# Kernel tuning notes

Measured on AMD Instinct MI355X. Metric: run time of the kernel, lower is better.

The kernel has to match this reference:

```python
import jax, jax.numpy as jnp
import numpy as np
from jax import lax

NB, D_MODEL, D_INNER, D_STATE, K, L, BATCH, NCLS, DT_RANK = 3, 512, 1024, 8, 4, 2048, 4, 10, 32


def setup_inputs() -> dict:
    key = jax.random.key(0)
    ks = jax.random.split(key, 12)
    s = 0.02
    inp = {
        "x": jax.random.normal(ks[0], (BATCH, L, D_MODEL), jnp.float32),
        "in_proj_w": s * jax.random.normal(ks[1], (NB, D_MODEL, 2 * D_INNER), jnp.float32),
        "conv_w": s * jax.random.normal(ks[2], (NB, D_INNER, K), jnp.float32),
        "conv_b": jnp.zeros((NB, D_INNER), jnp.float32),
        "x_proj_w": s * jax.random.normal(ks[3], (NB, D_INNER, DT_RANK + 2 * D_STATE), jnp.float32),
        "dt_proj_w": s * jax.random.normal(ks[4], (NB, DT_RANK, D_INNER), jnp.float32),
        "dt_proj_b": jnp.full((NB, D_INNER), -4.0, jnp.float32),
        "A_log": jnp.broadcast_to(jnp.log(jnp.arange(1, D_STATE + 1, dtype=jnp.float32)), (NB, D_INNER, D_STATE)).copy(),
        "D": jnp.ones((NB, D_INNER), jnp.float32),
        "out_proj_w": s * jax.random.normal(ks[5], (NB, D_INNER, D_MODEL), jnp.float32),
        "cls_w": s * jax.random.normal(ks[6], (D_MODEL, NCLS), jnp.float32),
        "cls_b": jnp.zeros((NCLS,), jnp.float32),
    }
    return inp


def _mamba_block(x, Wi, cw, cb, Wx, Wdt, bdt, A_log, Dp, Wo):
    # x: [B, L, d_model]
    Bsz, Lx, _ = x.shape
    d_inner = Dp.shape[0]
    d_state = A_log.shape[-1]
    dt_rank = Wdt.shape[0]
    xz = x @ Wi                               # [B, L, 2*d_inner]
    u, z = jnp.split(xz, 2, axis=-1)
    # causal depthwise conv1d over time
    uc = jnp.swapaxes(u, 1, 2)                # [B, d_inner, L]
    k = cw.shape[-1]
    uc = lax.conv_general_dilated(uc, cw[:, None, :], window_strides=(1,),
                                  padding=[(k - 1, 0)], feature_group_count=d_inner,
                                  dimension_numbers=("NCH", "OIH", "NCH"))
    u = jax.nn.silu(jnp.swapaxes(uc, 1, 2) + cb)   # [B, L, d_inner]
    dbl = u @ Wx                                   # [B, L, dt_rank + 2*d_state]
    dt = dbl[..., :dt_rank]
    Bm = dbl[..., dt_rank:dt_rank + d_state]
    Cm = dbl[..., dt_rank + d_state:]
    delta = jax.nn.softplus(dt @ Wdt + bdt)        # [B, L, d_inner]
    A = -jnp.exp(A_log)                            # [d_inner, d_state]

    def step(h, inp):
        d_t, B_t, C_t, u_t = inp                   # [B,d],[B,n],[B,n],[B,d]
        h = jnp.exp(d_t[..., None] * A) * h + (d_t * u_t)[..., None] * B_t[:, None, :]
        return h, jnp.einsum("bdn,bn->bd", h, C_t)

    xs = (jnp.swapaxes(delta, 0, 1), jnp.swapaxes(Bm, 0, 1),
          jnp.swapaxes(Cm, 0, 1), jnp.swapaxes(u, 0, 1))
    h0 = jnp.zeros((Bsz, d_inner, d_state), x.dtype)
    _, ys = lax.scan(step, h0, xs)                 # ys: [L, B, d_inner]
    y = jnp.swapaxes(ys, 0, 1) + u * Dp
    y = y * jax.nn.silu(z)
    return x + y @ Wo                              # residual


def reference(x, in_proj_w, conv_w, conv_b, x_proj_w, dt_proj_w, dt_proj_b, A_log, D, out_proj_w, cls_w, cls_b):
    nb = in_proj_w.shape[0]
    for i in range(nb):
        x = _mamba_block(x, in_proj_w[i], conv_w[i], conv_b[i], x_proj_w[i],
                         dt_proj_w[i], dt_proj_b[i], A_log[i], D[i], out_proj_w[i])
    pooled = jnp.mean(x, axis=1)                   # AdaptiveAvgPool1d(1) over seq
    return pooled @ cls_w + cls_b                  # [B, num_classes]
```

## Files before the change

### kernel.cpp

```cpp
#include <hip/hip_runtime.h>
#include <cstddef>
#include <cstdint>

#define L_SEQ   2048
#define BATCH_N 4
#define DMODEL  512
#define DINNER  1024
#define DSTATE  8
#define KCONV   4
#define DTRANK  32
#define NBLK    3
#define NCLS_N  10
#define MROWS   (BATCH_N * L_SEQ)
#define DBLW    48
#define NSPLIT  8

#define LC2 16
#define NC2 (L_SEQ / LC2)
#define DHALF (DINNER / 2)
#define SCAN_THREADS 512
#define SCAN_WAVES   (SCAN_THREADS / 64)

#define CGRP 8
#define CPG  (NC2 / CGRP)

typedef __attribute__((ext_vector_type(8))) short bf16x8;
typedef __attribute__((ext_vector_type(4))) short bf16x4;
typedef __attribute__((ext_vector_type(2))) short bf16x2;
typedef __attribute__((ext_vector_type(4))) float f32x4;

__device__ __forceinline__ float sigmoid_fast(float x) { return 1.f / (1.f + __expf(-x)); }
__device__ __forceinline__ float silu_fast(float x)    { return x * sigmoid_fast(x); }
__device__ __forceinline__ float softplus_fast(float x){
    return fmaxf(x, 0.f) + __logf(1.f + __expf(-fabsf(x)));
}
__device__ __forceinline__ float exp2_fast(float x) {
#if __has_builtin(__builtin_amdgcn_exp2f)
    return __builtin_amdgcn_exp2f(x);
#else
    return __expf(x * 0.69314718055994531f);
#endif
}
#define LOG2E 1.44269504088896341f

__device__ __forceinline__ unsigned short f2bf(float f) {
    union { float f; uint32_t u; } v; v.f = f;
    const uint32_t u = v.u;
    return (unsigned short)((u + 0x7fffu + ((u >> 16) & 1u)) >> 16);
}
__device__ __forceinline__ float bf2f(unsigned short h) {
    union { uint32_t u; float f; } v; v.u = ((uint32_t)h) << 16;
    return v.f;
}
__device__ __forceinline__ float bf2f_s(short h) { return bf2f((unsigned short)h); }

__device__ __forceinline__ void load_lds16(const void* g, void* l) {
    __builtin_amdgcn_global_load_lds(
        (const __attribute__((address_space(1))) unsigned int*)g,
        (__attribute__((address_space(3))) unsigned int*)l,
        16, 0, 0);
}

template <int K, int NT, int EPI>
__global__ __launch_bounds__(256) void gemm_bf16(
    const unsigned short* __restrict__ A, int lda,
    const unsigned short* __restrict__ Bt, int ldb,
    int ldc,
    unsigned short* __restrict__ Obf,
    float* __restrict__ pool)
{
    constexpr int BCH   = NT / 8;
    constexpr int NTW   = NT / 32;
    constexpr int STAGE = 8192 + NT * 64;
    constexpr int EPIL  = 128 * (NT + 8);
    constexpr int SMEM  = (STAGE > EPIL) ? STAGE : EPIL;
    __shared__ unsigned short sMem[SMEM];
    unsigned short* sA = sMem;
    unsigned short* sB = sMem + 8192;

    const int tid  = threadIdx.x;
    const int lane = tid & 63;
    const int wave = tid >> 6;
    const int m0 = blockIdx.y * 128;
    const int n0 = blockIdx.x * NT;
    const int wm = (wave >> 1) * 64;
    const int wn = (wave & 1) * (NT / 2);
    const int lm = lane & 15;
    const int lq = lane >> 4;

    const int srow = lane >> 3;
    const int scol = ((lane & 7) ^ srow) * 8;

    f32x4 acc[4][NTW];
    #pragma unroll
    for (int i = 0; i < 4; ++i)
        #pragma unroll
        for (int j = 0; j < NTW; ++j) acc[i][j] = (f32x4){0.f, 0.f, 0.f, 0.f};

    for (int k0 = 0; k0 < K; k0 += 64) {
        #pragma unroll
        for (int c = wave; c < 16; c += 4)
            load_lds16(A + (size_t)(m0 + c * 8 + srow) * lda + k0 + scol, &sA[c * 512]);
        #pragma unroll
        for (int c = wave; c < BCH; c += 4)
            load_lds16(Bt + (size_t)(n0 + c * 8 + srow) * ldb + k0 + scol, &sB[c * 512]);
        __syncthreads();
        #pragma unroll
        for (int ks = 0; ks < 2; ++ks) {
            bf16x8 aF[4], bF[NTW];
            #pragma unroll
            for (int mt = 0; mt < 4; ++mt) {
                const int row = wm + mt * 16 + lm;
                aF[mt] = *(const bf16x8*)&sA[row * 64 + (((ks * 4 + lq) ^ (lm & 7)) * 8)];
            }
            #pragma unroll
            for (int nt = 0; nt < NTW; ++nt) {
                const int row = wn + nt * 16 + lm;
                bF[nt] = *(const bf16x8*)&sB[row * 64 + (((ks * 4 + lq) ^ (lm & 7)) * 8)];
            }
            #pragma unroll
            for (int mt = 0; mt < 4; ++mt)
                #pragma unroll
                for (int nt = 0; nt < NTW; ++nt)
                    acc[mt][nt] = __builtin_amdgcn_mfma_f32_16x16x32_bf16(
                        aF[mt], bF[nt], acc[mt][nt], 0, 0, 0);
        }
        __syncthreads();
    }

    unsigned short* sOut = sMem;
    #pragma unroll
    for (int mt = 0; mt < 4; ++mt) {
        #pragma unroll
        for (int nt = 0; nt < NTW; ++nt) {
            #pragma unroll
            for (int r = 0; r < 4; ++r) {
                const int row = wm + mt * 16 + lq * 4 + r;
                const int col = wn + nt * 16 + lm;
                float v = acc[mt][nt][r];
                if (EPI >= 2) {
                    const size_t gi = (size_t)(m0 + row) * ldc + n0 + col;
                    v += bf2f(Obf[gi]);
                }
                sOut[row * (NT + 8) + col] = f2bf(v);
            }
        }
    }
    __syncthreads();
    #pragma unroll
    for (int j = 0; j < NT / 16; ++j) {
        const int idx = j * 256 + tid;
        const int row = idx / (NT / 8);
        const int cpos = (idx % (NT / 8)) * 8;
        *(bf16x8*)&Obf[(size_t)(m0 + row) * ldc + n0 + cpos] =
            *(const bf16x8*)&sOut[row * (NT + 8) + cpos];
    }
    if (EPI == 3) {
        const int b = m0 >> 11;
        const int col = tid & (NT - 1);
        const int q = tid / NT;
        constexpr int RPQ = 128 / (256 / NT);
        float s = 0.f;
        #pragma unroll
        for (int r = q * RPQ; r < (q + 1) * RPQ; ++r)
            s += bf2f(sOut[r * (NT + 8) + col]);
        atomicAdd(&pool[b * DMODEL + n0 + col], s);
    }
}

__global__ __launch_bounds__(256) void gemm_xproj(
    const unsigned short* __restrict__ ub,
    const unsigned short* __restrict__ Wxt,
    float* __restrict__ Xp)
{
    const int tid = threadIdx.x, lane = tid & 63, wave = tid >> 6;
    const int lm = lane & 15, lq = lane >> 4;
    const int rowA = blockIdx.x * 128 + wave * 32;
    const int split = blockIdx.y;
    const int k0 = split * (DINNER / NSPLIT);

    f32x4 acc[2][3];
    #pragma unroll
    for (int i = 0; i < 2; ++i)
        #pragma unroll
        for (int j = 0; j < 3; ++j) acc[i][j] = (f32x4){0.f, 0.f, 0.f, 0.f};

    #pragma unroll
    for (int kk = 0; kk < DINNER / NSPLIT; kk += 32) {
        const int k = k0 + kk;
        bf16x8 aF[2], bF[3];
        #pragma unroll
        for (int mt = 0; mt < 2; ++mt)
            aF[mt] = *(const bf16x8*)&ub[(size_t)(rowA + mt * 16 + lm) * DINNER + k + lq * 8];
        #pragma unroll
        for (int nt = 0; nt < 3; ++nt)
            bF[nt] = *(const bf16x8*)&Wxt[(size_t)(nt * 16 + lm) * DINNER + k + lq * 8];
        #pragma unroll
        for (int mt = 0; mt < 2; ++mt)
            #pragma unroll
            for (int nt = 0; nt < 3; ++nt)
                acc[mt][nt] = __builtin_amdgcn_mfma_f32_16x16x32_bf16(
                    aF[mt], bF[nt], acc[mt][nt], 0, 0, 0);
    }
    float* dst = Xp + (size_t)split * MROWS * DBLW;
    #pragma unroll
    for (int mt = 0; mt < 2; ++mt)
        #pragma unroll
        for (int nt = 0; nt < 3; ++nt)
            #pragma unroll
            for (int r = 0; r < 4; ++r)
                dst[(size_t)(rowA + mt * 16 + lq * 4 + r) * DBLW
                    + nt * 16 + lm] = acc[mt][nt][r];
}

__global__ __launch_bounds__(256) void xp_reduce(
    const float* __restrict__ Xp, float* __restrict__ dblsum)
{
    const int i = blockIdx.x * 256 + threadIdx.x;
    f32x4 s = (f32x4){0.f, 0.f, 0.f, 0.f};
    #pragma unroll
    for (int sp = 0; sp < NSPLIT; ++sp)
        s += ((const f32x4*)(Xp + (size_t)sp * MROWS * DBLW))[i];
    ((f32x4*)dblsum)[i] = s;
}

__global__ void prep_negA(const float* __restrict__ A_log, float* __restrict__ negA) {
    const int i = blockIdx.x * 256 + threadIdx.x;
    if (i < NBLK * DINNER * DSTATE)
        negA[i] = -__expf(A_log[i]) * LOG2E;
}

__global__ __launch_bounds__(256) void transpose_cast(
    const float* __restrict__ in, unsigned short* __restrict__ out,
    int Kdim, int Ndim, size_t in_stride, size_t out_stride)
{
    __shared__ float s[32][33];
    const float* ip = in + blockIdx.z * in_stride;
    unsigned short* op = out + blockIdx.z * out_stride;
    const int bx = blockIdx.x * 32;
    const int by = blockIdx.y * 32;
    const int t = threadIdx.x;
    const int r = t >> 3;
    const int c4 = (t & 7) * 4;

    const int row = by + r;
    if (bx + c4 + 3 < Ndim) {
        float4 v = *(const float4*)&ip[(size_t)row * Ndim + bx + c4];
        s[r][c4 + 0] = v.x; s[r][c4 + 1] = v.y; s[r][c4 + 2] = v.z; s[r][c4 + 3] = v.w;
    } else {
        for (int i = 0; i < 4; ++i) {
            const int col = bx + c4 + i;
            s[r][c4 + i] = (col < Ndim) ? ip[(size_t)row * Ndim + col] : 0.f;
        }
    }
    __syncthreads();
    if (bx + r < Ndim) {
        unsigned short w0 = f2bf(s[c4 + 0][r]), w1 = f2bf(s[c4 + 1][r]);
        unsigned short w2 = f2bf(s[c4 + 2][r]), w3 = f2bf(s[c4 + 3][r]);
        uint2 pk;
        pk.x = (uint32_t)w0 | ((uint32_t)w1 << 16);
        pk.y = (uint32_t)w2 | ((uint32_t)w3 << 16);
        *(uint2*)&op[(size_t)(bx + r) * Kdim + by + c4] = pk;
    }
}

__global__ void cast_init(const float* __restrict__ in, unsigned short* __restrict__ outb,
                          float* __restrict__ pooled_accum, int n4) {
    const int i = blockIdx.x * 256 + threadIdx.x;
    if (i < BATCH_N * DMODEL / 4)
        ((f32x4*)pooled_accum)[i] = (f32x4){0.f, 0.f, 0.f, 0.f};
    if (i >= n4) return;
    float4 v = ((const float4*)in)[i];
    uint2 pk;
    pk.x = (uint32_t)f2bf(v.x) | ((uint32_t)f2bf(v.y) << 16);
    pk.y = (uint32_t)f2bf(v.z) | ((uint32_t)f2bf(v.w) << 16);
    ((uint2*)outb)[i] = pk;
}

__global__ void conv_w_transpose(const float* __restrict__ cw, float* __restrict__ cwt) {
    const int i = blockIdx.x * 256 + threadIdx.x;
    if (i >= NBLK * DINNER * KCONV) return;
    const int blk = i >> 12;
    const int rem = i & 4095;
    const int d = rem >> 2;
    const int k = rem & 3;
    cwt[blk * 4096 + k * DINNER + d] = cw[blk * 4096 + d * KCONV + k];
}

__global__ __launch_bounds__(256) void conv_silu_kernel(
    const unsigned short* __restrict__ xz,
    const float* __restrict__ cwt,
    const float* __restrict__ cb,
    unsigned short* __restrict__ ub)
{
    const int idx = blockIdx.x * 256 + threadIdx.x;
    const int dv = idx & 127;
    const int m  = idx >> 7;
    const int t  = m & (L_SEQ - 1);
    const int d0 = dv * 8;

    float acc[8];
    {
        float4 c0 = *(const float4*)&cb[d0];
        float4 c1 = *(const float4*)&cb[d0 + 4];
        acc[0] = c0.x; acc[1] = c0.y; acc[2] = c0.z; acc[3] = c0.w;
        acc[4] = c1.x; acc[5] = c1.y; acc[6] = c1.z; acc[7] = c1.w;
    }
    #pragma unroll
    for (int k = 0; k < KCONV; ++k) {
        const int tt = t + k - (KCONV - 1);
        if (tt >= 0) {
            bf16x8 xv = *(const bf16x8*)&xz[(size_t)(m - t + tt) * (2 * DINNER) + d0];
            float4 w0 = *(const float4*)&cwt[k * DINNER + d0];
            float4 w1 = *(const float4*)&cwt[k * DINNER + d0 + 4];
            acc[0] = fmaf(bf2f_s(xv[0]), w0.x, acc[0]);
            acc[1] = fmaf(bf2f_s(xv[1]), w0.y, acc[1]);
            acc[2] = fmaf(bf2f_s(xv[2]), w0.z, acc[2]);
            acc[3] = fmaf(bf2f_s(xv[3]), w0.w, acc[3]);
            acc[4] = fmaf(bf2f_s(xv[4]), w1.x, acc[4]);
            acc[5] = fmaf(bf2f_s(xv[5]), w1.y, acc[5]);
            acc[6] = fmaf(bf2f_s(xv[6]), w1.z, acc[6]);
            acc[7] = fmaf(bf2f_s(xv[7]), w1.w, acc[7]);
        }
    }
    bf16x8 o;
    #pragma unroll
    for (int j = 0; j < 8; ++j) o[j] = (short)f2bf(silu_fast(acc[j]));
    *(bf16x8*)&ub[(size_t)m * DINNER + d0] = o;
}

__device__ __forceinline__ void dt_recompute_lds(
    unsigned short* sDelta,
    const float* __restrict__ dblsum,
    const unsigned short* __restrict__ Wdtt,
    const float* __restrict__ bdt,
    size_t m0, int lane, int wave, int dbase)
{
    const int lm = lane & 15, lq = lane >> 4;
    bf16x8 aF;
    {
        const float* p = &dblsum[(m0 + lm) * DBLW + lq * 8];
        float4 x0 = *(const float4*)p;
        float4 x1 = *(const float4*)(p + 4);
        aF[0] = (short)f2bf(x0.x); aF[1] = (short)f2bf(x0.y);
        aF[2] = (short)f2bf(x0.z); aF[3] = (short)f2bf(x0.w);
        aF[4] = (short)f2bf(x1.x); aF[5] = (short)f2bf(x1.y);
        aF[6] = (short)f2bf(x1.z); aF[7] = (short)f2bf(x1.w);
    }
    constexpr int NPW = DHALF / (16 * SCAN_WAVES);
    #pragma unroll
    for (int nt = 0; nt < NPW; ++nt) {
        const int cloc = wave * (DHALF / SCAN_WAVES) + nt * 16;
        const int col16 = dbase + cloc;
        bf16x8 bF = *(const bf16x8*)&Wdtt[(size_t)(col16 + lm) * DTRANK + lq * 8];
        f32x4 acc = (f32x4){0.f, 0.f, 0.f, 0.f};
        acc = __builtin_amdgcn_mfma_f32_16x16x32_bf16(aF, bF, acc, 0, 0, 0);
        const float bias = bdt[col16 + lm];
        #pragma unroll
        for (int r = 0; r < 4; ++r)
            sDelta[(lq * 4 + r) * DHALF + cloc + lm] =
                f2bf(softplus_fast(acc[r] + bias));
    }
}

__global__ __launch_bounds__(SCAN_THREADS) void scan_chunk_kernel(
    const unsigned short* __restrict__ ub,
    const float* __restrict__ dblsum,
    const unsigned short* __restrict__ Wdtt,
    const float* __restrict__ bdt,
    const float* __restrict__ negA,
    float* __restrict__ PSbuf)
{
    const int c  = blockIdx.x;
    const int dh = blockIdx.y;
    const int b  = blockIdx.z;
    const int tid = threadIdx.x;
    const int lane = tid & 63;
    const int wave = tid >> 6;
    const int dbase = dh * DHALF;
    const int d = dbase + tid;

    __shared__ unsigned short sDelta[LC2 * DHALF];
    __shared__ float sB[LC2][DSTATE];

    const size_t m0 = (size_t)b * L_SEQ + c * LC2;

    dt_recompute_lds(sDelta, dblsum, Wdtt, bdt, m0, lane, wave, dbase);
    if (tid < LC2 * DSTATE) {
        const int r = tid >> 3, n = tid & 7;
        sB[r][n] = dblsum[(m0 + r) * DBLW + DTRANK + n];
    }
    __syncthreads();

    float a[DSTATE], S[DSTATE];
    {
        float4 a0 = *(const float4*)&negA[(size_t)d * DSTATE];
        float4 a1 = *(const float4*)&negA[(size_t)d * DSTATE + 4];
        a[0] = a0.x; a[1] = a0.y; a[2] = a0.z; a[3] = a0.w;
        a[4] = a1.x; a[5] = a1.y; a[6] = a1.z; a[7] = a1.w;
    }
    #pragma unroll
    for (int n = 0; n < DSTATE; ++n) S[n] = 0.f;
    float dtsum = 0.f;

    for (int r = 0; r < LC2; ++r) {
        const size_t m = m0 + r;
        const float dt = bf2f(sDelta[r * DHALF + tid]);
        const float du = dt * bf2f(ub[m * DINNER + d]);
        dtsum += dt;
        #pragma unroll
        for (int n = 0; n < DSTATE; ++n) {
            const float e = exp2_fast(dt * a[n]);
            S[n] = fmaf(e, S[n], du * sB[r][n]);
        }
    }

    const size_t nb = (size_t)(b * NC2 + c) * DSTATE;
    #pragma unroll
    for (int n = 0; n < DSTATE; ++n) {
        float2 ps;
        ps.x = exp2_fast(a[n] * dtsum);
        ps.y = S[n];
        *(float2*)&PSbuf[(nb + n) * (DINNER * 2) + (size_t)d * 2] = ps;
    }
}

__global__ __launch_bounds__(512) void scan_combine_kernel(
    const float* __restrict__ PSbuf,
    float* __restrict__ Hbuf)
{
    const int dl = threadIdx.x & 63;
    const int g  = threadIdx.x >> 6;
    const int d  = blockIdx.x * 64 + dl;
    const int n  = blockIdx.y;
    const int b  = blockIdx.z;

    __shared__ float sP[CGRP][64];
    __shared__ float sS[CGRP][64];

    const int c0 = g * CPG;
    float Pseg = 1.f, Sseg = 0.f;
    #pragma unroll 4
    for (int cc = 0; cc < CPG; ++cc) {
        const size_t row = (size_t)(b * NC2 + c0 + cc) * DSTATE + n;
        const float2 ps = *(const float2*)&PSbuf[row * (DINNER * 2) + (size_t)d * 2];
        Pseg *= ps.x;
        Sseg = fmaf(ps.x, Sseg, ps.y);
    }
    sP[g][dl] = Pseg;
    sS[g][dl] = Sseg;
    __syncthreads();

    float h = 0.f;
    for (int gg = 0; gg < g; ++gg)
        h = fmaf(sP[gg][dl], h, sS[gg][dl]);

    #pragma unroll 4
    for (int cc = 0; cc < CPG; ++cc) {
        const size_t row = (size_t)(b * NC2 + c0 + cc) * DSTATE + n;
        const float2 ps = *(const float2*)&PSbuf[row * (DINNER * 2) + (size_t)d * 2];
        Hbuf[row * DINNER + d] = h;
        h = fmaf(ps.x, h, ps.y);
    }
}

__global__ __launch_bounds__(SCAN_THREADS) void scan_out_kernel(
    const unsigned short* __restrict__ ub,
    const float* __restrict__ dblsum,
    const unsigned short* __restrict__ Wdtt,
    const float* __restrict__ bdt,
    const unsigned short* __restrict__ xz,
    const float* __restrict__ negA,
    const float* __restrict__ Dp,
    const float* __restrict__ Hin,
    unsigned short* __restrict__ ybuf)
{
    const int c  = blockIdx.x;
    const int dh = blockIdx.y;
    const int b  = blockIdx.z;
    const int tid = threadIdx.x;
    const int lane = tid & 63;
    const int wave = tid >> 6;
    const int dbase = dh * DHALF;
    const int d = dbase + tid;

    __shared__ unsigned short sDelta[LC2 * DHALF];
    __shared__ float sB[LC2][DSTATE];
    __shared__ float sC[LC2][DSTATE];

    const size_t m0 = (size_t)b * L_SEQ + c * LC2;

    dt_recompute_lds(sDelta, dblsum, Wdtt, bdt, m0, lane, wave, dbase);
    if (tid < LC2 * 2 * DSTATE) {
        const int r = tid >> 4, j = tid & 15;
        const float v = dblsum[(m0 + r) * DBLW + DTRANK + j];
        if (j < DSTATE) sB[r][j] = v;
        else            sC[r][j - DSTATE] = v;
    }
    __syncthreads();

    float a[DSTATE], h[DSTATE];
    {
        float4 a0 = *(const float4*)&negA[(size_t)d * DSTATE];
        float4 a1 = *(const float4*)&negA[(size_t)d * DSTATE + 4];
        a[0] = a0.x; a[1] = a0.y; a[2] = a0.z; a[3] = a0.w;
        a[4] = a1.x; a[5] = a1.y; a[6] = a1.z; a[7] = a1.w;
    }
    const size_t base = ((size_t)(b * NC2 + c) * DSTATE) * DINNER + d;
    #pragma unroll
    for (int n = 0; n < DSTATE; ++n)
        h[n] = Hin[base + (size_t)n * DINNER];
    const float Dd = Dp[d];

    for (int r = 0; r < LC2; ++r) {
        const size_t m = m0 + r;
        const float dt = bf2f(sDelta[r * DHALF + tid]);
        const float ut = bf2f(ub[m * DINNER + d]);
        const float zt = bf2f(xz[m * (2 * DINNER) + DINNER + d]);
        const float du = dt * ut;
        float acc = 0.f;
        #pragma unroll
        for (int n = 0; n < DSTATE; ++n) {
            const float e = exp2_fast(dt * a[n]);
            h[n] = fmaf(e, h[n], du * sB[r][n]);
            acc = fmaf(h[n], sC[r][n], acc);
        }
        ybuf[m * DINNER + d] = f2bf(fmaf(ut, Dd, acc) * silu_fast(zt));
    }
}

__global__ __launch_bounds__(512) void pool_cls_kernel(
    const float* __restrict__ pooled_accum,
    const float* __restrict__ w,
    const float* __restrict__ bias,
    float* __restrict__ out)
{
    __shared__ float sp[DMODEL];
    const int b = blockIdx.x;
    const int dm = threadIdx.x;
    sp[dm] = pooled_accum[b * DMODEL + dm] * (1.f / (float)L_SEQ);
    __syncthreads();
    if (dm < NCLS_N) {
        float acc = bias[dm];
        for (int k = 0; k < DMODEL; ++k)
            acc = fmaf(sp[k], w[k * NCLS_N + dm], acc);
        out[b * NCLS_N + dm] = acc;
    }
}

extern "C" void kernel_launch(void* const* d_in, const int* in_sizes, int n_in,
                              void* d_out, int out_size, void* d_ws, size_t ws_size,
                              hipStream_t stream) {
    const float* x_in      = (const float*)d_in[0];
    const float* in_proj_w = (const float*)d_in[1];
    const float* conv_w    = (const float*)d_in[2];
    const float* conv_b    = (const float*)d_in[3];
    const float* x_proj_w  = (const float*)d_in[4];
    const float* dt_proj_w = (const float*)d_in[5];
    const float* dt_proj_b = (const float*)d_in[6];
    const float* A_log     = (const float*)d_in[7];
    const float* Dp        = (const float*)d_in[8];
    const float* out_proj_w= (const float*)d_in[9];
    const float* cls_w     = (const float*)d_in[10];
    const float* cls_b     = (const float*)d_in[11];
    float* out = (float*)d_out;

    char* w = (char*)d_ws;
    auto alloc = [&](size_t bytes) { char* p = w; w += (bytes + 255) & ~(size_t)255; return p; };
    unsigned short* xz_bf  = (unsigned short*)alloc((size_t)MROWS * 2 * DINNER * 2);
    unsigned short* ub     = (unsigned short*)alloc((size_t)MROWS * DINNER * 2);
    float*          Xp     = (float*)         alloc((size_t)NSPLIT * MROWS * DBLW * 4);
    float*          dblsum = (float*)         alloc((size_t)MROWS * DBLW * 4);
    float*          PSbuf  = (float*)         alloc((size_t)BATCH_N * NC2 * DSTATE * DINNER * 2 * 4);
    float*          Hbuf   = (float*)         alloc((size_t)BATCH_N * NC2 * DSTATE * DINNER * 4);
    unsigned short* xb     = (unsigned short*)alloc((size_t)MROWS * DMODEL * 2);
    unsigned short* ybuf   = (unsigned short*)alloc((size_t)MROWS * DINNER * 2);
    unsigned short* Wit    = (unsigned short*)alloc((size_t)NBLK * 2048 * 512 * 2);
    unsigned short* Wot    = (unsigned short*)alloc((size_t)NBLK * 512 * 1024 * 2);
    unsigned short* Wxt    = (unsigned short*)alloc((size_t)NBLK * DBLW * 1024 * 2);
    unsigned short* Wdtt   = (unsigned short*)alloc((size_t)NBLK * 1024 * DTRANK * 2);
    float*          cwt    = (float*)         alloc((size_t)NBLK * KCONV * DINNER * 4);
    float*          negA   = (float*)         alloc((size_t)NBLK * DINNER * DSTATE * 4);
    float*          pooled = (float*)         alloc((size_t)BATCH_N * DMODEL * 4);

    cast_init<<<(MROWS * DMODEL / 4) / 256, 256, 0, stream>>>(
        x_in, xb, pooled, MROWS * DMODEL / 4);
    transpose_cast<<<dim3(2048 / 32, 512 / 32, NBLK), 256, 0, stream>>>(
        in_proj_w, Wit, 512, 2048, (size_t)512 * 2048, (size_t)2048 * 512);
    transpose_cast<<<dim3(512 / 32, 1024 / 32, NBLK), 256, 0, stream>>>(
        out_proj_w, Wot, 1024, 512, (size_t)1024 * 512, (size_t)512 * 1024);
    transpose_cast<<<dim3(2, 1024 / 32, NBLK), 256, 0, stream>>>(
        x_proj_w, Wxt, 1024, DBLW, (size_t)1024 * DBLW, (size_t)DBLW * 1024);
    transpose_cast<<<dim3(1024 / 32, 1, NBLK), 256, 0, stream>>>(
        dt_proj_w, Wdtt, DTRANK, 1024, (size_t)DTRANK * 1024, (size_t)1024 * DTRANK);
    conv_w_transpose<<<(NBLK * DINNER * KCONV + 255) / 256, 256, 0, stream>>>(conv_w, cwt);
    prep_negA<<<(NBLK * DINNER * DSTATE + 255) / 256, 256, 0, stream>>>(A_log, negA);

    for (int blk = 0; blk < NBLK; ++blk) {
        const unsigned short* Wit_b  = Wit  + (size_t)blk * 2048 * 512;
        const unsigned short* Wot_b  = Wot  + (size_t)blk * 512 * 1024;
        const unsigned short* Wxt_b  = Wxt  + (size_t)blk * DBLW * 1024;
        const unsigned short* Wdtt_b = Wdtt + (size_t)blk * 1024 * DTRANK;
        const float* cwt_b = cwt + (size_t)blk * KCONV * DINNER;
        const float* cb  = conv_b    + (size_t)blk * DINNER;
        const float* bdt = dt_proj_b + (size_t)blk * DINNER;
        const float* nA  = negA      + (size_t)blk * DINNER * DSTATE;
        const float* Dv  = Dp        + (size_t)blk * DINNER;

        gemm_bf16<512, 128, 0><<<dim3(2048 / 128, MROWS / 128), 256, 0, stream>>>(
            xb, DMODEL, Wit_b, DMODEL, 2 * DINNER, xz_bf, nullptr);
        conv_silu_kernel<<<(MROWS * 128) / 256, 256, 0, stream>>>(
            xz_bf, cwt_b, cb, ub);
        gemm_xproj<<<dim3(MROWS / 128, NSPLIT), 256, 0, stream>>>(ub, Wxt_b, Xp);
        xp_reduce<<<(MROWS * DBLW / 4) / 256, 256, 0, stream>>>(Xp, dblsum);
        {
            dim3 gridA(NC2, 2, BATCH_N);
            scan_chunk_kernel<<<gridA, SCAN_THREADS, 0, stream>>>(
                ub, dblsum, Wdtt_b, bdt, nA, PSbuf);
            scan_combine_kernel<<<dim3(DINNER / 64, DSTATE, BATCH_N), 512, 0, stream>>>(
                PSbuf, Hbuf);
            scan_out_kernel<<<gridA, SCAN_THREADS, 0, stream>>>(
                ub, dblsum, Wdtt_b, bdt, xz_bf, nA, Dv, Hbuf, ybuf);
        }
        if (blk < NBLK - 1)
            gemm_bf16<1024, 64, 2><<<dim3(DMODEL / 64, MROWS / 128), 256, 0, stream>>>(
                ybuf, DINNER, Wot_b, DINNER, DMODEL, xb, nullptr);
        else
            gemm_bf16<1024, 64, 3><<<dim3(DMODEL / 64, MROWS / 128), 256, 0, stream>>>(
                ybuf, DINNER, Wot_b, DINNER, DMODEL, xb, pooled);
    }

    pool_cls_kernel<<<BATCH_N, DMODEL, 0, stream>>>(pooled, cls_w, cls_b, out);
}
```

Measured before the change: 521.5 us.

## Fuse chunked scan, combine and output passes into one cooperative kernel

Merges the three scan kernels (chunk summary, cross-chunk combine, output) into a single cooperative launch separated by grid-wide syncs. The delta recompute and B/C loads into LDS now happen once instead of twice, and the u values are kept in registers between phases. This removes two kernel launches and the repeated delta GEMM and global reloads. In exchange, the whole 1024-block grid must be co-resident (launch bounds raised to 8 blocks per CU), grid syncs add latency, and the combine phase runs on only half the blocks.

```diff
diff --git a/kernel.cpp b/kernel.cpp
--- a/kernel.cpp
+++ b/kernel.cpp
@@ -1,6 +1,9 @@
 #include <hip/hip_runtime.h>
+#include <hip/hip_cooperative_groups.h>
 #include <cstddef>
 #include <cstdint>
+
+namespace cg = cooperative_groups;
 
 #define L_SEQ   2048
 #define BATCH_N 4
@@ -363,13 +366,17 @@
     }
 }
 
-__global__ __launch_bounds__(SCAN_THREADS) void scan_chunk_kernel(
+__global__ __launch_bounds__(SCAN_THREADS, 8) void scan_fused(
     const unsigned short* __restrict__ ub,
     const float* __restrict__ dblsum,
     const unsigned short* __restrict__ Wdtt,
     const float* __restrict__ bdt,
+    const unsigned short* __restrict__ xz,
     const float* __restrict__ negA,
-    float* __restrict__ PSbuf)
+    const float* __restrict__ Dp,
+    float* __restrict__ PSbuf,
+    float* __restrict__ Hbuf,
+    unsigned short* __restrict__ ybuf)
 {
     const int c  = blockIdx.x;
     const int dh = blockIdx.y;
@@ -382,111 +389,9 @@
 
     __shared__ unsigned short sDelta[LC2 * DHALF];
     __shared__ float sB[LC2][DSTATE];
-
-    const size_t m0 = (size_t)b * L_SEQ + c * LC2;
-
-    dt_recompute_lds(sDelta, dblsum, Wdtt, bdt, m0, lane, wave, dbase);
-    if (tid < LC2 * DSTATE) {
-        const int r = tid >> 3, n = tid & 7;
-        sB[r][n] = dblsum[(m0 + r) * DBLW + DTRANK + n];
-    }
-    __syncthreads();
-
-    float a[DSTATE], S[DSTATE];
-    {
-        float4 a0 = *(const float4*)&negA[(size_t)d * DSTATE];
-        float4 a1 = *(const float4*)&negA[(size_t)d * DSTATE + 4];
-        a[0] = a0.x; a[1] = a0.y; a[2] = a0.z; a[3] = a0.w;
-        a[4] = a1.x; a[5] = a1.y; a[6] = a1.z; a[7] = a1.w;
-    }
-    #pragma unroll
-    for (int n = 0; n < DSTATE; ++n) S[n] = 0.f;
-    float dtsum = 0.f;
-
-    for (int r = 0; r < LC2; ++r) {
-        const size_t m = m0 + r;
-        const float dt = bf2f(sDelta[r * DHALF + tid]);
-        const float du = dt * bf2f(ub[m * DINNER + d]);
-        dtsum += dt;
-        #pragma unroll
-        for (int n = 0; n < DSTATE; ++n) {
-            const float e = exp2_fast(dt * a[n]);
-            S[n] = fmaf(e, S[n], du * sB[r][n]);
-        }
-    }
-
-    const size_t nb = (size_t)(b * NC2 + c) * DSTATE;
-    #pragma unroll
-    for (int n = 0; n < DSTATE; ++n) {
-        float2 ps;
-        ps.x = exp2_fast(a[n] * dtsum);
-        ps.y = S[n];
-        *(float2*)&PSbuf[(nb + n) * (DINNER * 2) + (size_t)d * 2] = ps;
-    }
-}
-
-__global__ __launch_bounds__(512) void scan_combine_kernel(
-    const float* __restrict__ PSbuf,
-    float* __restrict__ Hbuf)
-{
-    const int dl = threadIdx.x & 63;
-    const int g  = threadIdx.x >> 6;
-    const int d  = blockIdx.x * 64 + dl;
-    const int n  = blockIdx.y;
-    const int b  = blockIdx.z;
-
+    __shared__ float sC[LC2][DSTATE];
     __shared__ float sP[CGRP][64];
     __shared__ float sS[CGRP][64];
-
-    const int c0 = g * CPG;
-    float Pseg = 1.f, Sseg = 0.f;
-    #pragma unroll 4
-    for (int cc = 0; cc < CPG; ++cc) {
-        const size_t row = (size_t)(b * NC2 + c0 + cc) * DSTATE + n;
-        const float2 ps = *(const float2*)&PSbuf[row * (DINNER * 2) + (size_t)d * 2];
-        Pseg *= ps.x;
-        Sseg = fmaf(ps.x, Sseg, ps.y);
-    }
-    sP[g][dl] = Pseg;
-    sS[g][dl] = Sseg;
-    __syncthreads();
-
-    float h = 0.f;
-    for (int gg = 0; gg < g; ++gg)
-        h = fmaf(sP[gg][dl], h, sS[gg][dl]);
-
-    #pragma unroll 4
-    for (int cc = 0; cc < CPG; ++cc) {
-        const size_t row = (size_t)(b * NC2 + c0 + cc) * DSTATE + n;
-        const float2 ps = *(const float2*)&PSbuf[row * (DINNER * 2) + (size_t)d * 2];
-        Hbuf[row * DINNER + d] = h;
-        h = fmaf(ps.x, h, ps.y);
-    }
-}
-
-__global__ __launch_bounds__(SCAN_THREADS) void scan_out_kernel(
-    const unsigned short* __restrict__ ub,
-    const float* __restrict__ dblsum,
-    const unsigned short* __restrict__ Wdtt,
-    const float* __restrict__ bdt,
-    const unsigned short* __restrict__ xz,
-    const float* __restrict__ negA,
-    const float* __restrict__ Dp,
-    const float* __restrict__ Hin,
-    unsigned short* __restrict__ ybuf)
-{
-    const int c  = blockIdx.x;
-    const int dh = blockIdx.y;
-    const int b  = blockIdx.z;
-    const int tid = threadIdx.x;
-    const int lane = tid & 63;
-    const int wave = tid >> 6;
-    const int dbase = dh * DHALF;
-    const int d = dbase + tid;
-
-    __shared__ unsigned short sDelta[LC2 * DHALF];
-    __shared__ float sB[LC2][DSTATE];
-    __shared__ float sC[LC2][DSTATE];
 
     const size_t m0 = (size_t)b * L_SEQ + c * LC2;
 
@@ -499,33 +404,104 @@
     }
     __syncthreads();
 
-    float a[DSTATE], h[DSTATE];
+    float a[DSTATE];
     {
         float4 a0 = *(const float4*)&negA[(size_t)d * DSTATE];
         float4 a1 = *(const float4*)&negA[(size_t)d * DSTATE + 4];
         a[0] = a0.x; a[1] = a0.y; a[2] = a0.z; a[3] = a0.w;
         a[4] = a1.x; a[5] = a1.y; a[6] = a1.z; a[7] = a1.w;
     }
-    const size_t base = ((size_t)(b * NC2 + c) * DSTATE) * DINNER + d;
-    #pragma unroll
-    for (int n = 0; n < DSTATE; ++n)
-        h[n] = Hin[base + (size_t)n * DINNER];
-    const float Dd = Dp[d];
-
-    for (int r = 0; r < LC2; ++r) {
-        const size_t m = m0 + r;
-        const float dt = bf2f(sDelta[r * DHALF + tid]);
-        const float ut = bf2f(ub[m * DINNER + d]);
-        const float zt = bf2f(xz[m * (2 * DINNER) + DINNER + d]);
-        const float du = dt * ut;
-        float acc = 0.f;
+
+    uint32_t upk[LC2 / 2];
+    {
+        float S[DSTATE];
+        #pragma unroll
+        for (int n = 0; n < DSTATE; ++n) S[n] = 0.f;
+        float dtsum = 0.f;
+        for (int r = 0; r < LC2; ++r) {
+            const size_t m = m0 + r;
+            const unsigned short ubits = ub[m * DINNER + d];
+            if (r & 1) upk[r >> 1] |= ((uint32_t)ubits << 16);
+            else       upk[r >> 1]  = (uint32_t)ubits;
+            const float dt = bf2f(sDelta[r * DHALF + tid]);
+            const float du = dt * bf2f(ubits);
+            dtsum += dt;
+            #pragma unroll
+            for (int n = 0; n < DSTATE; ++n) {
+                const float e = exp2_fast(dt * a[n]);
+                S[n] = fmaf(e, S[n], du * sB[r][n]);
+            }
+        }
+        const size_t nb = (size_t)(b * NC2 + c) * DSTATE;
         #pragma unroll
         for (int n = 0; n < DSTATE; ++n) {
-            const float e = exp2_fast(dt * a[n]);
-            h[n] = fmaf(e, h[n], du * sB[r][n]);
-            acc = fmaf(h[n], sC[r][n], acc);
-        }
-        ybuf[m * DINNER + d] = f2bf(fmaf(ut, Dd, acc) * silu_fast(zt));
+            float2 ps;
+            ps.x = exp2_fast(a[n] * dtsum);
+            ps.y = S[n];
+            *(float2*)&PSbuf[(nb + n) * (DINNER * 2) + (size_t)d * 2] = ps;
+        }
+    }
+
+    cg::this_grid().sync();
+
+    {
+        const int flat = c + NC2 * (dh + 2 * b);
+        if (flat < 512) {
+            const int bx = flat & 15;
+            const int n2 = (flat >> 4) & 7;
+            const int b2 = flat >> 7;
+            const int dl = tid & 63;
+            const int g  = tid >> 6;
+            const int dd = bx * 64 + dl;
+            const int c0 = g * CPG;
+            float Pseg = 1.f, Sseg = 0.f;
+            #pragma unroll 4
+            for (int cc = 0; cc < CPG; ++cc) {
+                const size_t row = (size_t)(b2 * NC2 + c0 + cc) * DSTATE + n2;
+                const float2 ps = *(const float2*)&PSbuf[row * (DINNER * 2) + (size_t)dd * 2];
+                Pseg *= ps.x;
+                Sseg = fmaf(ps.x, Sseg, ps.y);
+            }
+            sP[g][dl] = Pseg;
+            sS[g][dl] = Sseg;
+            __syncthreads();
+            float h = 0.f;
+            for (int gg = 0; gg < g; ++gg)
+                h = fmaf(sP[gg][dl], h, sS[gg][dl]);
+            #pragma unroll 4
+            for (int cc = 0; cc < CPG; ++cc) {
+                const size_t row = (size_t)(b2 * NC2 + c0 + cc) * DSTATE + n2;
+                const float2 ps = *(const float2*)&PSbuf[row * (DINNER * 2) + (size_t)dd * 2];
+                Hbuf[row * DINNER + dd] = h;
+                h = fmaf(ps.x, h, ps.y);
+            }
+        }
+    }
+
+    cg::this_grid().sync();
+
+    {
+        float h[DSTATE];
+        const size_t base = ((size_t)(b * NC2 + c) * DSTATE) * DINNER + d;
+        #pragma unroll
+        for (int n = 0; n < DSTATE; ++n)
+            h[n] = Hbuf[base + (size_t)n * DINNER];
+        const float Dd = Dp[d];
+        for (int r = 0; r < LC2; ++r) {
+            const size_t m = m0 + r;
+            const float dt = bf2f(sDelta[r * DHALF + tid]);
+            const float ut = bf2f((unsigned short)((upk[r >> 1] >> ((r & 1) * 16)) & 0xffffu));
+            const float zt = bf2f(xz[m * (2 * DINNER) + DINNER + d]);
+            const float du = dt * ut;
+            float acc = 0.f;
+            #pragma unroll
+            for (int n = 0; n < DSTATE; ++n) {
+                const float e = exp2_fast(dt * a[n]);
+                h[n] = fmaf(e, h[n], du * sB[r][n]);
+                acc = fmaf(h[n], sC[r][n], acc);
+            }
+            ybuf[m * DINNER + d] = f2bf(fmaf(ut, Dd, acc) * silu_fast(zt));
+        }
     }
 }
 
@@ -614,13 +590,21 @@
         gemm_xproj<<<dim3(MROWS / 128, NSPLIT), 256, 0, stream>>>(ub, Wxt_b, Xp);
         xp_reduce<<<(MROWS * DBLW / 4) / 256, 256, 0, stream>>>(Xp, dblsum);
         {
-            dim3 gridA(NC2, 2, BATCH_N);
-            scan_chunk_kernel<<<gridA, SCAN_THREADS, 0, stream>>>(
-                ub, dblsum, Wdtt_b, bdt, nA, PSbuf);
-            scan_combine_kernel<<<dim3(DINNER / 64, DSTATE, BATCH_N), 512, 0, stream>>>(
-                PSbuf, Hbuf);
-            scan_out_kernel<<<gridA, SCAN_THREADS, 0, stream>>>(
-                ub, dblsum, Wdtt_b, bdt, xz_bf, nA, Dv, Hbuf, ybuf);
+            const unsigned short* ub_p   = ub;
+            const float*          dbl_p  = dblsum;
+            const unsigned short* wdtt_p = Wdtt_b;
+            const float*          bdt_p  = bdt;
+            const unsigned short* xz_p   = xz_bf;
+            const float*          na_p   = nA;
+            const float*          dp_p   = Dv;
+            float*                ps_p   = PSbuf;
+            float*                h_p    = Hbuf;
+            unsigned short*       y_p    = ybuf;
+            void* kargs[] = {&ub_p, &dbl_p, &wdtt_p, &bdt_p, &xz_p,
+                             &na_p, &dp_p, &ps_p, &h_p, &y_p};
+            hipLaunchCooperativeKernel((const void*)scan_fused,
+                                       dim3(NC2, 2, BATCH_N), dim3(SCAN_THREADS),
+                                       kargs, 0, stream);
         }
         if (blk < NBLK - 1)
             gemm_bf16<1024, 64, 2><<<dim3(DMODEL / 64, MROWS / 128), 256, 0, stream>>>(
```

Measured after the change: 1.297 ms. 2.49x slower.

## Remap GEMM workgroups per XCD and halve xproj tile rows

Applied to the files above, without the earlier changes.

The main bf16 GEMM now remaps its flat workgroup index so that consecutive tiles land on the same XCD (MI355X dispatches workgroups round-robin across 8 XCDs). The aim is better L2 reuse of shared A/B panels. Separately, gemm_xproj now uses 16 rows per wave instead of 32 and launches twice as many blocks, trading register reuse of B fragments for more parallelism and occupancy. The remap assumes the round-robin dispatch order and adds a little index arithmetic.

```diff
diff --git a/kernel.cpp b/kernel.cpp
--- a/kernel.cpp
+++ b/kernel.cpp
@@ -81,8 +81,18 @@
     const int tid  = threadIdx.x;
     const int lane = tid & 63;
     const int wave = tid >> 6;
-    const int m0 = blockIdx.y * 128;
-    const int n0 = blockIdx.x * NT;
+
+    const int nwgx = gridDim.x;
+    const int nwg  = nwgx * gridDim.y;
+    int flat = blockIdx.y * nwgx + blockIdx.x;
+    {
+        const int q = nwg >> 3, r = nwg & 7;
+        const int xcd = flat & 7, lid = flat >> 3;
+        flat = (xcd < r ? xcd * (q + 1) : r * (q + 1) + (xcd - r) * q) + lid;
+    }
+    const int m0 = (flat / nwgx) * 128;
+    const int n0 = (flat % nwgx) * NT;
+
     const int wm = (wave >> 1) * 64;
     const int wn = (wave & 1) * (NT / 2);
     const int lm = lane & 15;
@@ -175,42 +185,33 @@
 {
     const int tid = threadIdx.x, lane = tid & 63, wave = tid >> 6;
     const int lm = lane & 15, lq = lane >> 4;
-    const int rowA = blockIdx.x * 128 + wave * 32;
+    const int rowA = blockIdx.x * 64 + wave * 16;
     const int split = blockIdx.y;
     const int k0 = split * (DINNER / NSPLIT);
 
-    f32x4 acc[2][3];
-    #pragma unroll
-    for (int i = 0; i < 2; ++i)
-        #pragma unroll
-        for (int j = 0; j < 3; ++j) acc[i][j] = (f32x4){0.f, 0.f, 0.f, 0.f};
+    f32x4 acc[3];
+    #pragma unroll
+    for (int j = 0; j < 3; ++j) acc[j] = (f32x4){0.f, 0.f, 0.f, 0.f};
 
     #pragma unroll
     for (int kk = 0; kk < DINNER / NSPLIT; kk += 32) {
         const int k = k0 + kk;
-        bf16x8 aF[2], bF[3];
-        #pragma unroll
-        for (int mt = 0; mt < 2; ++mt)
-            aF[mt] = *(const bf16x8*)&ub[(size_t)(rowA + mt * 16 + lm) * DINNER + k + lq * 8];
+        bf16x8 aF = *(const bf16x8*)&ub[(size_t)(rowA + lm) * DINNER + k + lq * 8];
+        bf16x8 bF[3];
         #pragma unroll
         for (int nt = 0; nt < 3; ++nt)
             bF[nt] = *(const bf16x8*)&Wxt[(size_t)(nt * 16 + lm) * DINNER + k + lq * 8];
         #pragma unroll
-        for (int mt = 0; mt < 2; ++mt)
-            #pragma unroll
-            for (int nt = 0; nt < 3; ++nt)
-                acc[mt][nt] = __builtin_amdgcn_mfma_f32_16x16x32_bf16(
-                    aF[mt], bF[nt], acc[mt][nt], 0, 0, 0);
+        for (int nt = 0; nt < 3; ++nt)
+            acc[nt] = __builtin_amdgcn_mfma_f32_16x16x32_bf16(
+                aF, bF[nt], acc[nt], 0, 0, 0);
     }
     float* dst = Xp + (size_t)split * MROWS * DBLW;
     #pragma unroll
-    for (int mt = 0; mt < 2; ++mt)
-        #pragma unroll
-        for (int nt = 0; nt < 3; ++nt)
-            #pragma unroll
-            for (int r = 0; r < 4; ++r)
-                dst[(size_t)(rowA + mt * 16 + lq * 4 + r) * DBLW
-                    + nt * 16 + lm] = acc[mt][nt][r];
+    for (int nt = 0; nt < 3; ++nt)
+        #pragma unroll
+        for (int r = 0; r < 4; ++r)
+            dst[(size_t)(rowA + lq * 4 + r) * DBLW + nt * 16 + lm] = acc[nt][r];
 }
 
 __global__ __launch_bounds__(256) void xp_reduce(
@@ -611,7 +612,7 @@
             xb, DMODEL, Wit_b, DMODEL, 2 * DINNER, xz_bf, nullptr);
         conv_silu_kernel<<<(MROWS * 128) / 256, 256, 0, stream>>>(
             xz_bf, cwt_b, cb, ub);
-        gemm_xproj<<<dim3(MROWS / 128, NSPLIT), 256, 0, stream>>>(ub, Wxt_b, Xp);
+        gemm_xproj<<<dim3(MROWS / 64, NSPLIT), 256, 0, stream>>>(ub, Wxt_b, Xp);
         xp_reduce<<<(MROWS * DBLW / 4) / 256, 256, 0, stream>>>(Xp, dblsum);
         {
             dim3 gridA(NC2, 2, BATCH_N);
```

New measurement: 507.2 us. 1.03x faster.
